# Performance work log

Measured on AMD Instinct MI355X. Metric: run time of the kernel, lower is better.

## Reference

```python
import jax, jax.numpy as jnp
import numpy as np

S, B, D = 1024, 32, 1024

def setup_inputs() -> dict:
    key = jax.random.key(0)
    k1, k2, k3, k4, k5 = jax.random.split(key, 5)
    x = jax.random.normal(k1, (S, B, D), dtype=jnp.float32)
    layer_input = jax.random.normal(k2, (S, B, D), dtype=jnp.float32)
    position_embedding = jax.random.normal(k3, (S, B, D), dtype=jnp.float32)
    # pad indicator == 1 (True); random pads, ~half the positions
    encoder_mask = jax.random.randint(k4, (B, S), 0, 2).astype(bool)
    W = jax.random.normal(k5, (D, 1), dtype=jnp.float32) * (1.0 / np.sqrt(D))
    b = jnp.zeros((1,), dtype=jnp.float32)
    return {"x": x, "layer_input": layer_input,
            "position_embedding": position_embedding,
            "encoder_mask": encoder_mask, "W": W, "b": b}

def reference(x, layer_input, position_embedding, encoder_mask, W, b):
    s, bsz, d = x.shape
    valid = (~encoder_mask).astype(x.dtype)            # (B, S)
    sentence_length = valid.sum(axis=-1)               # (B,)
    langtok_index = s - sentence_length                # (B,)
    # predicted soft position in [0, sentence_length]
    pred = jax.nn.sigmoid(x @ W + b)[..., 0]           # (S, B)
    pred = pred * sentence_length[None, :]             # (S, B)
    # absolute positions shifted by language-token offset
    all_pos = jnp.arange(s, dtype=x.dtype)[:, None] - langtok_index[None, :]  # (S, B)
    # distances[i, b, j] = pred[i, b] - all_pos[j, b]
    dist = pred[:, :, None] - all_pos.T[None, :, :]    # (S, B, S)
    prob = 1.0 / (dist * dist + 0.001)                 # reciprocal squared distance
    prob = prob * valid[None, :, :]                    # zero out pads along j
    prob = prob / prob.sum(axis=-1, keepdims=True)     # normalize over source positions
    # weighted sum of position embeddings: (S,B,S) x (S,B,D) -> (S,B,D)
    out = jnp.einsum('ibj,jbd->ibd', prob, position_embedding)
    out = out * valid.T[:, :, None]                    # zero out pad rows
    return out
```

## Files before the change

kernel.cpp:

```cpp
#include <hip/hip_runtime.h>


#define S_ 1024
#define B_ 32
#define D_ 1024

typedef unsigned short us;
typedef __attribute__((ext_vector_type(4))) unsigned short us4;
typedef __attribute__((ext_vector_type(4))) float f4;
typedef __attribute__((ext_vector_type(8))) short short8;

__device__ __forceinline__ float bf2f(us u){
  unsigned v = ((unsigned)u) << 16;
  float f;
  __builtin_memcpy(&f, &v, 4);
  return f;
}
__device__ __forceinline__ us f2bf(float f){
  unsigned v;
  __builtin_memcpy(&v, &f, 4);
  v = v + 0x7fffu + ((v >> 16) & 1u);
  return (us)(v >> 16);
}

__device__ __forceinline__ void gll16(const void* g, void* l){
  __builtin_amdgcn_global_load_lds(
      (const __attribute__((address_space(1))) void*)g,
      (__attribute__((address_space(3))) void*)l,
      16, 0, 0);
}

__global__ __launch_bounds__(256) void prep_k(const unsigned char* __restrict__ mask,
                                              float* __restrict__ valid,
                                              float* __restrict__ slen,
                                              float* __restrict__ ltok)
{
  const int b = blockIdx.x;
  const int t = threadIdx.x;
  __shared__ int flags[5];
  __shared__ int red[256];
  if (t < 5) flags[t] = 0;
  __syncthreads();
  for (int k = 0; k < 32; ++k){
    int p = t * 32 + k;
    unsigned v = mask[p];
    if (v){
      atomicOr(&flags[p & 3], 1);
      if (v > 1u) atomicOr(&flags[4], 1);
    }
  }
  __syncthreads();
  int fmt;
  int any123 = flags[1] | flags[2] | flags[3];
  if (!flags[4]) fmt = any123 ? 0 : 1;
  else           fmt = (flags[0] | flags[1]) ? 2 : 3;

  int cnt = 0;
#pragma unroll
  for (int q = 0; q < 4; ++q){
    int j = t + q * 256;
    size_t idx = (size_t)b * S_ + j;
    unsigned mv;
    if (fmt == 0)      mv = mask[idx];
    else if (fmt == 1) mv = ((const unsigned int*)mask)[idx];
    else if (fmt == 2) mv = ((const unsigned short*)mask)[idx];
    else               mv = ((const unsigned int*)mask)[idx] & 0x7fffffffu;
    valid[idx] = mv ? 0.0f : 1.0f;
    cnt += mv ? 0 : 1;
  }
  red[t] = cnt;
  __syncthreads();
  for (int s = 128; s > 0; s >>= 1){
    if (t < s) red[t] += red[t + s];
    __syncthreads();
  }
  if (t == 0){
    float cn = (float)red[0];
    slen[b] = cn;
    ltok[b] = (float)S_ - cn;
  }
}

__device__ __forceinline__ void rowk_body(int blk, const float* __restrict__ x,
                                          const float* __restrict__ Wp,
                                          const float* __restrict__ bp,
                                          const float* __restrict__ valid,
                                          const float* __restrict__ slen,
                                          const float* __restrict__ ltok,
                                          us* __restrict__ P,
                                          float* __restrict__ rs,
                                          float* __restrict__ c_arr,
                                          bool writeP)
{
  const int wid  = threadIdx.x >> 6;
  const int lane = threadIdx.x & 63;
  const int row  = blk * 4 + wid;
  const int b = row & (B_ - 1);
  const int i = row >> 5;

  const float4* xr = (const float4*)(x + (size_t)row * D_);
  const float4* wr = (const float4*)Wp;
  float acc = 0.f;
#pragma unroll
  for (int q = 0; q < 4; ++q){
    float4 xv = xr[q * 64 + lane];
    float4 wv = wr[q * 64 + lane];
    acc += xv.x * wv.x + xv.y * wv.y + xv.z * wv.z + xv.w * wv.w;
  }
#pragma unroll
  for (int off = 32; off > 0; off >>= 1) acc += __shfl_xor(acc, off);

  float z   = acc + bp[0];
  float sig = 1.f / (1.f + expf(-z));
  float c   = sig * slen[b] + ltok[b];

  const float4* vr = (const float4*)(valid + (size_t)b * S_);
  us4* Pr = (us4*)(P + ((size_t)b * S_ + i) * S_);
  float wsum = 0.f;
#pragma unroll
  for (int q = 0; q < 4; ++q){
    int idx = q * 64 + lane;
    float4 vv = vr[idx];
    float j0 = (float)(idx * 4);
    float d0 = c - j0;
    float d1 = c - (j0 + 1.f);
    float d2 = c - (j0 + 2.f);
    float d3 = c - (j0 + 3.f);
    us p0 = f2bf(vv.x / (d0 * d0 + 1e-3f));
    us p1 = f2bf(vv.y / (d1 * d1 + 1e-3f));
    us p2 = f2bf(vv.z / (d2 * d2 + 1e-3f));
    us p3 = f2bf(vv.w / (d3 * d3 + 1e-3f));
    if (writeP){
      us4 pv; pv.x = p0; pv.y = p1; pv.z = p2; pv.w = p3;
      Pr[idx] = pv;
    }
    wsum += bf2f(p0) + bf2f(p1) + bf2f(p2) + bf2f(p3);
  }
#pragma unroll
  for (int off = 32; off > 0; off >>= 1) wsum += __shfl_xor(wsum, off);

  if (lane == 0){
    float vi = valid[(size_t)b * S_ + i];
    rs[(size_t)b * S_ + i] = (vi != 0.f) ? (vi / wsum) : 0.f;
    c_arr[(size_t)b * S_ + i] = c;
  }
}

__device__ __forceinline__ void transp_body(int j0, int d0, int b,
                                            const float* __restrict__ pe,
                                            us* __restrict__ Etr,
                                            us* tile )
{
  const int t  = threadIdx.x;
  const int rr = t >> 4, cc = t & 15;
#pragma unroll
  for (int q = 0; q < 4; ++q){
    int j = q * 16 + rr;
    float4 v = *(const float4*)(pe + ((size_t)(j0 + j) * B_ + b) * D_ + d0 + cc * 4);
    us4 tv; tv.x = f2bf(v.x); tv.y = f2bf(v.y); tv.z = f2bf(v.z); tv.w = f2bf(v.w);
    *(us4*)&tile[j * 68 + cc * 4] = tv;
  }
  __syncthreads();
#pragma unroll
  for (int q = 0; q < 4; ++q){
    int d = q * 16 + rr;
    us4 v;
    v.x = tile[(cc * 4 + 0) * 68 + d];
    v.y = tile[(cc * 4 + 1) * 68 + d];
    v.z = tile[(cc * 4 + 2) * 68 + d];
    v.w = tile[(cc * 4 + 3) * 68 + d];
    *(us4*)(Etr + ((size_t)b * D_ + d0 + d) * S_ + j0 + cc * 4) = v;
  }
}

__global__ __launch_bounds__(256) void mid_k(const float* __restrict__ x,
                                             const float* __restrict__ Wp,
                                             const float* __restrict__ bp,
                                             const float* __restrict__ valid,
                                             const float* __restrict__ slen,
                                             const float* __restrict__ ltok,
                                             us* __restrict__ P,
                                             float* __restrict__ rs,
                                             float* __restrict__ c_arr,
                                             const float* __restrict__ pe,
                                             us* __restrict__ Etr)
{
  __shared__ us tile[64 * 68];
  const int bid = blockIdx.x;
  if (bid < (S_ * B_ / 4)){
    rowk_body(bid, x, Wp, bp, valid, slen, ltok, P, rs, c_arr, true);
  } else {
    int id2 = bid - (S_ * B_ / 4);
    int jt = id2 & 15;
    int dt = (id2 >> 4) & 15;
    int b  = id2 >> 8;
    transp_body(jt * 64, dt * 64, b, pe, Etr, tile);
  }
}

__global__ __launch_bounds__(512, 2) void gemm_k(const us* __restrict__ P,
                                                 const us* __restrict__ Etr,
                                                 const float* __restrict__ rs,
                                                 float* __restrict__ out)
{
  const int bid = blockIdx.x;
  const int xcd = bid & 7;
  const int s   = bid >> 3;
  const int b   = xcd * 4 + (s >> 4);
  const int t16 = s & 15;
  const int i0  = (t16 >> 2) * 256;
  const int n0  = (t16 & 3) * 256;

  const int tid  = threadIdx.x;
  const int wid  = tid >> 6;
  const int lane = tid & 63;
  const int wm = wid >> 2, wn = wid & 3;
  const int ml = lane & 15, quad = lane >> 4;

  __shared__ __align__(16) us lds[4][2][8192];

  const us* gsrc[2];
  {
    int p = tid;
    int r = p >> 2;
    int c = (p & 3) ^ ((r >> 1) & 3);
    gsrc[0] = P   + ((size_t)b * S_ + (i0 + r)) * S_ + c * 8;
    gsrc[1] = Etr + ((size_t)b * D_ + (n0 + r)) * S_ + c * 8;
  }
  const int dst0 = wid * 64 * 8;

  int aoff[8], boff[4];
#pragma unroll
  for (int mt = 0; mt < 8; ++mt){
    int r = wm * 128 + mt * 16 + ml;
    aoff[mt] = r * 32 + ((quad ^ ((r >> 1) & 3)) * 8);
  }
#pragma unroll
  for (int nt = 0; nt < 4; ++nt){
    int r = wn * 64 + nt * 16 + ml;
    boff[nt] = r * 32 + ((quad ^ ((r >> 1) & 3)) * 8);
  }

  f4 acc[8][4];
#pragma unroll
  for (int mt = 0; mt < 8; ++mt)
#pragma unroll
    for (int nt = 0; nt < 4; ++nt){
      f4 z = {0.0f, 0.0f, 0.0f, 0.0f};
      acc[mt][nt] = z;
    }

  auto STAGE = [&](int slot, int h, int kt){
    const us* g = gsrc[h] + kt * 32;
    us* l = &lds[slot][h][dst0];
    gll16(g,                 l);
    gll16(g + 128 * S_,      l + 4096);
  };

  STAGE(0, 0, 0); STAGE(0, 1, 0);
  STAGE(1, 0, 1); STAGE(1, 1, 1);
  STAGE(2, 0, 2); STAGE(2, 1, 2);
  asm volatile("s_waitcnt vmcnt(8)" ::: "memory");
  __builtin_amdgcn_s_barrier();
  asm volatile("" ::: "memory");

#pragma unroll 1
  for (int kt = 0; kt < 32; ++kt){
    const int sl  = kt & 3;
    const int st  = (kt + 3) & 3;
    const int ktn = (kt < 29) ? (kt + 3) : 31;
    const us* A = lds[sl][0];
    const us* B = lds[sl][1];
    short8 av[4], av2[4], bv[4];

#pragma unroll
    for (int mt = 0; mt < 4; ++mt) av[mt] = *(const short8*)&A[aoff[mt]];
#pragma unroll
    for (int nt = 0; nt < 4; ++nt) bv[nt] = *(const short8*)&B[boff[nt]];
    STAGE(st, 0, ktn);
    __builtin_amdgcn_s_setprio(1);
#pragma unroll
    for (int mt = 0; mt < 4; ++mt)
#pragma unroll
      for (int nt = 0; nt < 4; ++nt)
        acc[mt][nt] = __builtin_amdgcn_mfma_f32_16x16x32_bf16(av[mt], bv[nt], acc[mt][nt], 0, 0, 0);
    __builtin_amdgcn_s_setprio(0);

#pragma unroll
    for (int mt = 0; mt < 4; ++mt) av2[mt] = *(const short8*)&A[aoff[4 + mt]];
    STAGE(st, 1, ktn);
    __builtin_amdgcn_s_setprio(1);
#pragma unroll
    for (int mt = 0; mt < 4; ++mt)
#pragma unroll
      for (int nt = 0; nt < 4; ++nt)
        acc[4 + mt][nt] = __builtin_amdgcn_mfma_f32_16x16x32_bf16(av2[mt], bv[nt], acc[4 + mt][nt], 0, 0, 0);
    __builtin_amdgcn_s_setprio(0);

    asm volatile("s_waitcnt vmcnt(8)" ::: "memory");
    __builtin_amdgcn_s_barrier();
    asm volatile("" ::: "memory");
  }
  asm volatile("s_waitcnt vmcnt(0)" ::: "memory");

  const float* rsb = rs + (size_t)b * S_;
#pragma unroll
  for (int mt = 0; mt < 8; ++mt){
#pragma unroll
    for (int reg = 0; reg < 4; ++reg){
      int i = i0 + wm * 128 + mt * 16 + quad * 4 + reg;
      float rv = rsb[i];
      size_t ob = ((size_t)i * B_ + b) * D_;
#pragma unroll
      for (int nt = 0; nt < 4; ++nt){
        int d = n0 + wn * 64 + nt * 16 + ml;
        out[ob + d] = acc[mt][nt][reg] * rv;
      }
    }
  }
}

__global__ __launch_bounds__(256) void rowk_nb(const float* __restrict__ x,
                                               const float* __restrict__ Wp,
                                               const float* __restrict__ bp,
                                               const float* __restrict__ valid,
                                               const float* __restrict__ slen,
                                               const float* __restrict__ ltok,
                                               float* __restrict__ rs,
                                               float* __restrict__ c_arr)
{
  rowk_body(blockIdx.x, x, Wp, bp, valid, slen, ltok, nullptr, rs, c_arr, false);
}

__global__ __launch_bounds__(256) void slow_out_k(const float* __restrict__ pe,
                                                  const float* __restrict__ valid,
                                                  const float* __restrict__ c_arr,
                                                  const float* __restrict__ rs,
                                                  float* __restrict__ out)
{
  const int bid = blockIdx.x;
  const int b = bid & (B_ - 1);
  const int i = bid >> 5;
  const int t = threadIdx.x;
  __shared__ float sw[S_];
  float c  = c_arr[(size_t)b * S_ + i];
  float rv = rs[(size_t)b * S_ + i];
#pragma unroll
  for (int q = 0; q < 4; ++q){
    int j = t + q * 256;
    float d = c - (float)j;
    sw[j] = valid[(size_t)b * S_ + j] / (d * d + 1e-3f);
  }
  __syncthreads();
  float a0 = 0, a1 = 0, a2 = 0, a3 = 0;
  if (rv != 0.0f){
    for (int j = 0; j < S_; ++j){
      float wj = sw[j];
      const float* row = pe + ((size_t)j * B_ + b) * D_;
      a0 += wj * row[t];
      a1 += wj * row[t + 256];
      a2 += wj * row[t + 512];
      a3 += wj * row[t + 768];
    }
  }
  float* orow = out + ((size_t)i * B_ + b) * D_;
  orow[t]       = a0 * rv;
  orow[t + 256] = a1 * rv;
  orow[t + 512] = a2 * rv;
  orow[t + 768] = a3 * rv;
}

extern "C" void kernel_launch(void* const* d_in, const int* in_sizes, int n_in,
                              void* d_out, int out_size, void* d_ws, size_t ws_size,
                              hipStream_t stream)
{
  (void)in_sizes; (void)n_in; (void)out_size;
  const float* x  = (const float*)d_in[0];
  const float* pe = (const float*)d_in[2];
  const unsigned char* mask = (const unsigned char*)d_in[3];
  const float* Wp = (const float*)d_in[4];
  const float* bp = (const float*)d_in[5];
  float* out = (float*)d_out;
  char* ws = (char*)d_ws;

  const size_t offValid = 0;
  const size_t offRs    = offValid + (size_t)B_ * S_ * 4;
  const size_t offSlen  = offRs    + (size_t)B_ * S_ * 4;
  const size_t offLtok  = offSlen  + 128;
  const size_t offC     = offLtok  + 128;
  const size_t offP     = offC     + (size_t)B_ * S_ * 4;
  const size_t offE     = offP     + (size_t)B_ * S_ * S_ * 2;
  const size_t need     = offE     + (size_t)B_ * D_ * S_ * 2;

  float* valid = (float*)(ws + offValid);
  float* rs    = (float*)(ws + offRs);
  float* slen  = (float*)(ws + offSlen);
  float* ltok  = (float*)(ws + offLtok);
  float* c_arr = (float*)(ws + offC);
  us* P   = (us*)(ws + offP);
  us* Etr = (us*)(ws + offE);

  prep_k<<<B_, 256, 0, stream>>>(mask, valid, slen, ltok);
  if (ws_size >= need){
    mid_k<<<16384, 256, 0, stream>>>(x, Wp, bp, valid, slen, ltok, P, rs, c_arr, pe, Etr);
    gemm_k<<<512, 512, 0, stream>>>(P, Etr, rs, out);
  } else {
    rowk_nb<<<S_ * B_ / 4, 256, 0, stream>>>(x, Wp, bp, valid, slen, ltok, rs, c_arr);
    slow_out_k<<<S_ * B_, 256, 0, stream>>>(pe, valid, c_arr, rs, out);
  }
}
```

Measured before the change: 454.5 us.

## Split fused mid kernel, use fast reciprocal, and register-double-buffer GEMM fragments

The combined mid kernel is split into separate transpose and row kernels, removing the branchy dual-role kernel and its shared tile allocation from the row path. The row kernel uses the hardware approximate reciprocal instead of a full division when building the bf16 probability matrix. The GEMM main loop is rewritten to stage both operands together and prefetch the next k-step's fragments into a second register set while issuing MFMAs on the current set, aiming to hide LDS latency. This adds register pressure from the doubled fragments and an extra kernel launch, and the approximate reciprocal slightly changes numerics.

```diff
diff --git a/kernel.cpp b/kernel.cpp
--- a/kernel.cpp
+++ b/kernel.cpp
@@ -81,20 +81,50 @@
   }
 }
 
-__device__ __forceinline__ void rowk_body(int blk, const float* __restrict__ x,
-                                          const float* __restrict__ Wp,
-                                          const float* __restrict__ bp,
-                                          const float* __restrict__ valid,
-                                          const float* __restrict__ slen,
-                                          const float* __restrict__ ltok,
-                                          us* __restrict__ P,
-                                          float* __restrict__ rs,
-                                          float* __restrict__ c_arr,
-                                          bool writeP)
+__global__ __launch_bounds__(256) void transp_k(const float* __restrict__ pe,
+                                                us* __restrict__ Etr)
+{
+  __shared__ us tile[64 * 68];
+  const int id = blockIdx.x;
+  const int j0 = (id & 15) * 64;
+  const int d0 = ((id >> 4) & 15) * 64;
+  const int b  = id >> 8;
+
+  const int t  = threadIdx.x;
+  const int rr = t >> 4, cc = t & 15;
+#pragma unroll
+  for (int q = 0; q < 4; ++q){
+    int j = q * 16 + rr;
+    float4 v = *(const float4*)(pe + ((size_t)(j0 + j) * B_ + b) * D_ + d0 + cc * 4);
+    us4 tv; tv.x = f2bf(v.x); tv.y = f2bf(v.y); tv.z = f2bf(v.z); tv.w = f2bf(v.w);
+    *(us4*)&tile[j * 68 + cc * 4] = tv;
+  }
+  __syncthreads();
+#pragma unroll
+  for (int q = 0; q < 4; ++q){
+    int d = q * 16 + rr;
+    us4 v;
+    v.x = tile[(cc * 4 + 0) * 68 + d];
+    v.y = tile[(cc * 4 + 1) * 68 + d];
+    v.z = tile[(cc * 4 + 2) * 68 + d];
+    v.w = tile[(cc * 4 + 3) * 68 + d];
+    *(us4*)(Etr + ((size_t)b * D_ + d0 + d) * S_ + j0 + cc * 4) = v;
+  }
+}
+
+__global__ __launch_bounds__(256) void rowk_k(const float* __restrict__ x,
+                                              const float* __restrict__ Wp,
+                                              const float* __restrict__ bp,
+                                              const float* __restrict__ valid,
+                                              const float* __restrict__ slen,
+                                              const float* __restrict__ ltok,
+                                              us* __restrict__ P,
+                                              float* __restrict__ rs,
+                                              float* __restrict__ c_arr)
 {
   const int wid  = threadIdx.x >> 6;
   const int lane = threadIdx.x & 63;
-  const int row  = blk * 4 + wid;
+  const int row  = blockIdx.x * 4 + wid;
   const int b = row & (B_ - 1);
   const int i = row >> 5;
 
@@ -116,6 +146,186 @@
 
   const float4* vr = (const float4*)(valid + (size_t)b * S_);
   us4* Pr = (us4*)(P + ((size_t)b * S_ + i) * S_);
+  float wsum = 0.f;
+#pragma unroll
+  for (int q = 0; q < 4; ++q){
+    int idx = q * 64 + lane;
+    float4 vv = vr[idx];
+    float j0 = (float)(idx * 4);
+    float d0 = c - j0;
+    float d1 = c - (j0 + 1.f);
+    float d2 = c - (j0 + 2.f);
+    float d3 = c - (j0 + 3.f);
+    us p0 = f2bf(vv.x * __builtin_amdgcn_rcpf(d0 * d0 + 1e-3f));
+    us p1 = f2bf(vv.y * __builtin_amdgcn_rcpf(d1 * d1 + 1e-3f));
+    us p2 = f2bf(vv.z * __builtin_amdgcn_rcpf(d2 * d2 + 1e-3f));
+    us p3 = f2bf(vv.w * __builtin_amdgcn_rcpf(d3 * d3 + 1e-3f));
+    us4 pv; pv.x = p0; pv.y = p1; pv.z = p2; pv.w = p3;
+    Pr[idx] = pv;
+    wsum += bf2f(p0) + bf2f(p1) + bf2f(p2) + bf2f(p3);
+  }
+#pragma unroll
+  for (int off = 32; off > 0; off >>= 1) wsum += __shfl_xor(wsum, off);
+
+  if (lane == 0){
+    float vi = valid[(size_t)b * S_ + i];
+    rs[(size_t)b * S_ + i] = (vi != 0.f) ? (vi / wsum) : 0.f;
+    c_arr[(size_t)b * S_ + i] = c;
+  }
+}
+
+__global__ __launch_bounds__(512, 2) void gemm_k(const us* __restrict__ P,
+                                                 const us* __restrict__ Etr,
+                                                 const float* __restrict__ rs,
+                                                 float* __restrict__ out)
+{
+  const int bid = blockIdx.x;
+  const int xcd = bid & 7;
+  const int s   = bid >> 3;
+  const int b   = xcd * 4 + (s >> 4);
+  const int t16 = s & 15;
+  const int i0  = (t16 >> 2) * 256;
+  const int n0  = (t16 & 3) * 256;
+
+  const int tid  = threadIdx.x;
+  const int wid  = tid >> 6;
+  const int lane = tid & 63;
+  const int wm = wid >> 2, wn = wid & 3;
+  const int ml = lane & 15, quad = lane >> 4;
+
+  __shared__ __align__(16) us lds[4][2][8192];
+
+  const us* gsrc[2];
+  {
+    int p = tid;
+    int r = p >> 2;
+    int c = (p & 3) ^ ((r >> 1) & 3);
+    gsrc[0] = P   + ((size_t)b * S_ + (i0 + r)) * S_ + c * 8;
+    gsrc[1] = Etr + ((size_t)b * D_ + (n0 + r)) * S_ + c * 8;
+  }
+  const int dst0 = wid * 64 * 8;
+
+  int aoff[8], boff[4];
+#pragma unroll
+  for (int mt = 0; mt < 8; ++mt){
+    int r = wm * 128 + mt * 16 + ml;
+    aoff[mt] = r * 32 + ((quad ^ ((r >> 1) & 3)) * 8);
+  }
+#pragma unroll
+  for (int nt = 0; nt < 4; ++nt){
+    int r = wn * 64 + nt * 16 + ml;
+    boff[nt] = r * 32 + ((quad ^ ((r >> 1) & 3)) * 8);
+  }
+
+  f4 acc[8][4];
+#pragma unroll
+  for (int mt = 0; mt < 8; ++mt)
+#pragma unroll
+    for (int nt = 0; nt < 4; ++nt){
+      f4 z = {0.0f, 0.0f, 0.0f, 0.0f};
+      acc[mt][nt] = z;
+    }
+
+  auto STAGE = [&](int slot, int kt){
+    const us* gA = gsrc[0] + kt * 32;
+    const us* gB = gsrc[1] + kt * 32;
+    us* lA = &lds[slot][0][dst0];
+    us* lB = &lds[slot][1][dst0];
+    gll16(gA,            lA);
+    gll16(gA + 128 * S_, lA + 4096);
+    gll16(gB,            lB);
+    gll16(gB + 128 * S_, lB + 4096);
+  };
+  auto READF = [&](short8* f, int slot){
+    const us* A  = lds[slot][0];
+    const us* Bm = lds[slot][1];
+#pragma unroll
+    for (int mt = 0; mt < 8; ++mt) f[mt] = *(const short8*)&A[aoff[mt]];
+#pragma unroll
+    for (int nt = 0; nt < 4; ++nt) f[8 + nt] = *(const short8*)&Bm[boff[nt]];
+  };
+  auto MFMA32 = [&](const short8* f){
+    __builtin_amdgcn_s_setprio(1);
+#pragma unroll
+    for (int mt = 0; mt < 8; ++mt)
+#pragma unroll
+      for (int nt = 0; nt < 4; ++nt)
+        acc[mt][nt] = __builtin_amdgcn_mfma_f32_16x16x32_bf16(f[mt], f[8 + nt], acc[mt][nt], 0, 0, 0);
+    __builtin_amdgcn_s_setprio(0);
+  };
+  short8 fA[12], fB[12];
+  auto HALF = [&](int kt, short8* cur, short8* nxt){
+    asm volatile("s_waitcnt vmcnt(4)" ::: "memory");
+    asm volatile("s_waitcnt lgkmcnt(0)" ::: "memory");
+    __builtin_amdgcn_sched_barrier(0);
+    __builtin_amdgcn_s_barrier();
+    const int ktn = (kt + 3 < 32) ? (kt + 3) : 31;
+    STAGE((kt + 3) & 3, ktn);
+    READF(nxt, (kt + 1) & 3);
+    MFMA32(cur);
+  };
+
+  STAGE(0, 0); STAGE(1, 1); STAGE(2, 2);
+  asm volatile("s_waitcnt vmcnt(8)" ::: "memory");
+  __builtin_amdgcn_s_barrier();
+  READF(fA, 0);
+
+#pragma unroll 1
+  for (int kt = 0; kt < 32; kt += 2){
+    HALF(kt,     fA, fB);
+    HALF(kt + 1, fB, fA);
+  }
+  asm volatile("s_waitcnt vmcnt(0)" ::: "memory");
+
+  const float* rsb = rs + (size_t)b * S_;
+#pragma unroll
+  for (int mt = 0; mt < 8; ++mt){
+#pragma unroll
+    for (int reg = 0; reg < 4; ++reg){
+      int i = i0 + wm * 128 + mt * 16 + quad * 4 + reg;
+      float rv = rsb[i];
+      size_t ob = ((size_t)i * B_ + b) * D_;
+#pragma unroll
+      for (int nt = 0; nt < 4; ++nt){
+        int d = n0 + wn * 64 + nt * 16 + ml;
+        out[ob + d] = acc[mt][nt][reg] * rv;
+      }
+    }
+  }
+}
+
+__global__ __launch_bounds__(256) void rowk_nb(const float* __restrict__ x,
+                                               const float* __restrict__ Wp,
+                                               const float* __restrict__ bp,
+                                               const float* __restrict__ valid,
+                                               const float* __restrict__ slen,
+                                               const float* __restrict__ ltok,
+                                               float* __restrict__ rs,
+                                               float* __restrict__ c_arr)
+{
+  const int wid  = threadIdx.x >> 6;
+  const int lane = threadIdx.x & 63;
+  const int row  = blockIdx.x * 4 + wid;
+  const int b = row & (B_ - 1);
+  const int i = row >> 5;
+
+  const float4* xr = (const float4*)(x + (size_t)row * D_);
+  const float4* wr = (const float4*)Wp;
+  float acc = 0.f;
+#pragma unroll
+  for (int q = 0; q < 4; ++q){
+    float4 xv = xr[q * 64 + lane];
+    float4 wv = wr[q * 64 + lane];
+    acc += xv.x * wv.x + xv.y * wv.y + xv.z * wv.z + xv.w * wv.w;
+  }
+#pragma unroll
+  for (int off = 32; off > 0; off >>= 1) acc += __shfl_xor(acc, off);
+
+  float z   = acc + bp[0];
+  float sig = 1.f / (1.f + expf(-z));
+  float c   = sig * slen[b] + ltok[b];
+
+  const float4* vr = (const float4*)(valid + (size_t)b * S_);
   float wsum = 0.f;
 #pragma unroll
   for (int q = 0; q < 4; ++q){
@@ -130,10 +340,6 @@
     us p1 = f2bf(vv.y / (d1 * d1 + 1e-3f));
     us p2 = f2bf(vv.z / (d2 * d2 + 1e-3f));
     us p3 = f2bf(vv.w / (d3 * d3 + 1e-3f));
-    if (writeP){
-      us4 pv; pv.x = p0; pv.y = p1; pv.z = p2; pv.w = p3;
-      Pr[idx] = pv;
-    }
     wsum += bf2f(p0) + bf2f(p1) + bf2f(p2) + bf2f(p3);
   }
 #pragma unroll
@@ -144,192 +350,6 @@
     rs[(size_t)b * S_ + i] = (vi != 0.f) ? (vi / wsum) : 0.f;
     c_arr[(size_t)b * S_ + i] = c;
   }
-}
-
-__device__ __forceinline__ void transp_body(int j0, int d0, int b,
-                                            const float* __restrict__ pe,
-                                            us* __restrict__ Etr,
-                                            us* tile )
-{
-  const int t  = threadIdx.x;
-  const int rr = t >> 4, cc = t & 15;
-#pragma unroll
-  for (int q = 0; q < 4; ++q){
-    int j = q * 16 + rr;
-    float4 v = *(const float4*)(pe + ((size_t)(j0 + j) * B_ + b) * D_ + d0 + cc * 4);
-    us4 tv; tv.x = f2bf(v.x); tv.y = f2bf(v.y); tv.z = f2bf(v.z); tv.w = f2bf(v.w);
-    *(us4*)&tile[j * 68 + cc * 4] = tv;
-  }
-  __syncthreads();
-#pragma unroll
-  for (int q = 0; q < 4; ++q){
-    int d = q * 16 + rr;
-    us4 v;
-    v.x = tile[(cc * 4 + 0) * 68 + d];
-    v.y = tile[(cc * 4 + 1) * 68 + d];
-    v.z = tile[(cc * 4 + 2) * 68 + d];
-    v.w = tile[(cc * 4 + 3) * 68 + d];
-    *(us4*)(Etr + ((size_t)b * D_ + d0 + d) * S_ + j0 + cc * 4) = v;
-  }
-}
-
-__global__ __launch_bounds__(256) void mid_k(const float* __restrict__ x,
-                                             const float* __restrict__ Wp,
-                                             const float* __restrict__ bp,
-                                             const float* __restrict__ valid,
-                                             const float* __restrict__ slen,
-                                             const float* __restrict__ ltok,
-                                             us* __restrict__ P,
-                                             float* __restrict__ rs,
-                                             float* __restrict__ c_arr,
-                                             const float* __restrict__ pe,
-                                             us* __restrict__ Etr)
-{
-  __shared__ us tile[64 * 68];
-  const int bid = blockIdx.x;
-  if (bid < (S_ * B_ / 4)){
-    rowk_body(bid, x, Wp, bp, valid, slen, ltok, P, rs, c_arr, true);
-  } else {
-    int id2 = bid - (S_ * B_ / 4);
-    int jt = id2 & 15;
-    int dt = (id2 >> 4) & 15;
-    int b  = id2 >> 8;
-    transp_body(jt * 64, dt * 64, b, pe, Etr, tile);
-  }
-}
-
-__global__ __launch_bounds__(512, 2) void gemm_k(const us* __restrict__ P,
-                                                 const us* __restrict__ Etr,
-                                                 const float* __restrict__ rs,
-                                                 float* __restrict__ out)
-{
-  const int bid = blockIdx.x;
-  const int xcd = bid & 7;
-  const int s   = bid >> 3;
-  const int b   = xcd * 4 + (s >> 4);
-  const int t16 = s & 15;
-  const int i0  = (t16 >> 2) * 256;
-  const int n0  = (t16 & 3) * 256;
-
-  const int tid  = threadIdx.x;
-  const int wid  = tid >> 6;
-  const int lane = tid & 63;
-  const int wm = wid >> 2, wn = wid & 3;
-  const int ml = lane & 15, quad = lane >> 4;
-
-  __shared__ __align__(16) us lds[4][2][8192];
-
-  const us* gsrc[2];
-  {
-    int p = tid;
-    int r = p >> 2;
-    int c = (p & 3) ^ ((r >> 1) & 3);
-    gsrc[0] = P   + ((size_t)b * S_ + (i0 + r)) * S_ + c * 8;
-    gsrc[1] = Etr + ((size_t)b * D_ + (n0 + r)) * S_ + c * 8;
-  }
-  const int dst0 = wid * 64 * 8;
-
-  int aoff[8], boff[4];
-#pragma unroll
-  for (int mt = 0; mt < 8; ++mt){
-    int r = wm * 128 + mt * 16 + ml;
-    aoff[mt] = r * 32 + ((quad ^ ((r >> 1) & 3)) * 8);
-  }
-#pragma unroll
-  for (int nt = 0; nt < 4; ++nt){
-    int r = wn * 64 + nt * 16 + ml;
-    boff[nt] = r * 32 + ((quad ^ ((r >> 1) & 3)) * 8);
-  }
-
-  f4 acc[8][4];
-#pragma unroll
-  for (int mt = 0; mt < 8; ++mt)
-#pragma unroll
-    for (int nt = 0; nt < 4; ++nt){
-      f4 z = {0.0f, 0.0f, 0.0f, 0.0f};
-      acc[mt][nt] = z;
-    }
-
-  auto STAGE = [&](int slot, int h, int kt){
-    const us* g = gsrc[h] + kt * 32;
-    us* l = &lds[slot][h][dst0];
-    gll16(g,                 l);
-    gll16(g + 128 * S_,      l + 4096);
-  };
-
-  STAGE(0, 0, 0); STAGE(0, 1, 0);
-  STAGE(1, 0, 1); STAGE(1, 1, 1);
-  STAGE(2, 0, 2); STAGE(2, 1, 2);
-  asm volatile("s_waitcnt vmcnt(8)" ::: "memory");
-  __builtin_amdgcn_s_barrier();
-  asm volatile("" ::: "memory");
-
-#pragma unroll 1
-  for (int kt = 0; kt < 32; ++kt){
-    const int sl  = kt & 3;
-    const int st  = (kt + 3) & 3;
-    const int ktn = (kt < 29) ? (kt + 3) : 31;
-    const us* A = lds[sl][0];
-    const us* B = lds[sl][1];
-    short8 av[4], av2[4], bv[4];
-
-#pragma unroll
-    for (int mt = 0; mt < 4; ++mt) av[mt] = *(const short8*)&A[aoff[mt]];
-#pragma unroll
-    for (int nt = 0; nt < 4; ++nt) bv[nt] = *(const short8*)&B[boff[nt]];
-    STAGE(st, 0, ktn);
-    __builtin_amdgcn_s_setprio(1);
-#pragma unroll
-    for (int mt = 0; mt < 4; ++mt)
-#pragma unroll
-      for (int nt = 0; nt < 4; ++nt)
-        acc[mt][nt] = __builtin_amdgcn_mfma_f32_16x16x32_bf16(av[mt], bv[nt], acc[mt][nt], 0, 0, 0);
-    __builtin_amdgcn_s_setprio(0);
-
-#pragma unroll
-    for (int mt = 0; mt < 4; ++mt) av2[mt] = *(const short8*)&A[aoff[4 + mt]];
-    STAGE(st, 1, ktn);
-    __builtin_amdgcn_s_setprio(1);
-#pragma unroll
-    for (int mt = 0; mt < 4; ++mt)
-#pragma unroll
-      for (int nt = 0; nt < 4; ++nt)
-        acc[4 + mt][nt] = __builtin_amdgcn_mfma_f32_16x16x32_bf16(av2[mt], bv[nt], acc[4 + mt][nt], 0, 0, 0);
-    __builtin_amdgcn_s_setprio(0);
-
-    asm volatile("s_waitcnt vmcnt(8)" ::: "memory");
-    __builtin_amdgcn_s_barrier();
-    asm volatile("" ::: "memory");
-  }
-  asm volatile("s_waitcnt vmcnt(0)" ::: "memory");
-
-  const float* rsb = rs + (size_t)b * S_;
-#pragma unroll
-  for (int mt = 0; mt < 8; ++mt){
-#pragma unroll
-    for (int reg = 0; reg < 4; ++reg){
-      int i = i0 + wm * 128 + mt * 16 + quad * 4 + reg;
-      float rv = rsb[i];
-      size_t ob = ((size_t)i * B_ + b) * D_;
-#pragma unroll
-      for (int nt = 0; nt < 4; ++nt){
-        int d = n0 + wn * 64 + nt * 16 + ml;
-        out[ob + d] = acc[mt][nt][reg] * rv;
-      }
-    }
-  }
-}
-
-__global__ __launch_bounds__(256) void rowk_nb(const float* __restrict__ x,
-                                               const float* __restrict__ Wp,
-                                               const float* __restrict__ bp,
-                                               const float* __restrict__ valid,
-                                               const float* __restrict__ slen,
-                                               const float* __restrict__ ltok,
-                                               float* __restrict__ rs,
-                                               float* __restrict__ c_arr)
-{
-  rowk_body(blockIdx.x, x, Wp, bp, valid, slen, ltok, nullptr, rs, c_arr, false);
 }
 
 __global__ __launch_bounds__(256) void slow_out_k(const float* __restrict__ pe,
@@ -402,7 +422,8 @@
 
   prep_k<<<B_, 256, 0, stream>>>(mask, valid, slen, ltok);
   if (ws_size >= need){
-    mid_k<<<16384, 256, 0, stream>>>(x, Wp, bp, valid, slen, ltok, P, rs, c_arr, pe, Etr);
+    transp_k<<<8192, 256, 0, stream>>>(pe, Etr);
+    rowk_k<<<S_ * B_ / 4, 256, 0, stream>>>(x, Wp, bp, valid, slen, ltok, P, rs, c_arr);
     gemm_k<<<512, 512, 0, stream>>>(P, Etr, rs, out);
   } else {
     rowk_nb<<<S_ * B_ / 4, 256, 0, stream>>>(x, Wp, bp, valid, slen, ltok, rs, c_arr);
```

Result: no change. 463.4 us (+2.0%).
